# Kernel tuning notes

Hardware: AMD Instinct MI355X
Metric: run time of the kernel (lower is better)

Reference implementation:

```python
import jax, jax.numpy as jnp
import numpy as np

NEG = -1e9  # large negative for masked logits (TRT uses dtype min)

def _rotate_every_two(x):
    # pairs (x0,x1) -> (-x1, x0), interleaved along last dim
    xr = x.reshape(*x.shape[:-1], -1, 2)
    rot = jnp.stack([-xr[..., 1], xr[..., 0]], axis=-1)
    return rot.reshape(x.shape)

def _apply_rope(x, cos, sin):
    # rot_dim == cos.shape[-1]; here it equals the full inner dim
    rot_dim = cos.shape[-1]
    x_rot, x_pass = x[..., :rot_dim], x[..., rot_dim:]
    x_rot = x_rot * cos + _rotate_every_two(x_rot) * sin
    return jnp.concatenate([x_rot, x_pass], axis=-1) if x_pass.shape[-1] else x_rot

def setup_inputs() -> dict:
    key = jax.random.key(0)
    ks = jax.random.split(key, 12)
    B, N, D_MODEL, H, DH = 2, 2048, 1024, 16, 64
    INNER = H * DH
    x = jax.random.normal(ks[0], (B, N, D_MODEL), dtype=jnp.float32)
    # rope angles: build realistic cos/sin tables repeated per head
    pos = jnp.arange(N, dtype=jnp.float32)
    inv = 1.0 / (10000.0 ** (jnp.arange(0, DH, 2, dtype=jnp.float32) / DH))
    ang = pos[:, None] * inv[None, :]              # [N, DH/2]
    ang = jnp.repeat(ang, 2, axis=-1)              # [N, DH] interleaved pairs
    ang = jnp.tile(ang, (1, H))                    # [N, INNER]
    rope_cos = jnp.broadcast_to(jnp.cos(ang)[None], (B, N, INNER)).astype(jnp.float32)
    rope_sin = jnp.broadcast_to(jnp.sin(ang)[None], (B, N, INNER)).astype(jnp.float32)
    input_lengths = jax.random.randint(ks[1], (B,), N // 2, N + 1, dtype=jnp.int32)
    s = 1.0 / np.sqrt(D_MODEL)
    Wq = jax.random.normal(ks[2], (D_MODEL, INNER), dtype=jnp.float32) * s
    bq = jnp.zeros((INNER,), jnp.float32)
    Wk = jax.random.normal(ks[3], (D_MODEL, INNER), dtype=jnp.float32) * s
    bk = jnp.zeros((INNER,), jnp.float32)
    Wv = jax.random.normal(ks[4], (D_MODEL, INNER), dtype=jnp.float32) * s
    bv = jnp.zeros((INNER,), jnp.float32)
    Wo = jax.random.normal(ks[5], (INNER, D_MODEL), dtype=jnp.float32) * (1.0 / np.sqrt(INNER))
    bo = jnp.zeros((D_MODEL,), jnp.float32)
    return {"x": x, "rope_cos": rope_cos, "rope_sin": rope_sin,
            "input_lengths": input_lengths,
            "Wq": Wq, "bq": bq, "Wk": Wk, "bk": bk, "Wv": Wv, "bv": bv,
            "Wo": Wo, "bo": bo}

def reference(x, rope_cos, rope_sin, input_lengths, Wq, bq, Wk, bk, Wv, bv, Wo, bo):
    B, N, _ = x.shape
    H, DH = 16, 64
    q = x @ Wq + bq
    k = x @ Wk + bk
    v = x @ Wv + bv
    q = _apply_rope(q, rope_cos, rope_sin)
    k = _apply_rope(k, rope_cos, rope_sin)
    # split heads: [B,N,H,DH] -> [B,H,N,DH]
    q = q.reshape(B, N, H, DH).transpose(0, 2, 1, 3)
    k = k.reshape(B, N, H, DH).transpose(0, 2, 1, 3)
    v = v.reshape(B, N, H, DH).transpose(0, 2, 1, 3)
    # NOTE: faithful to the non-plugin source path, q is NOT pre-scaled
    scores = jnp.einsum('bhqd,bhkd->bhqk', q, k)
    key_mask = jnp.arange(N)[None, :] < input_lengths[:, None]  # [B,N]
    scores = scores + jnp.where(key_mask, 0.0, NEG).astype(scores.dtype)[:, None, None, :]
    probs = jax.nn.softmax(scores, axis=-1)
    ctx = jnp.einsum('bhqk,bhkd->bhqd', probs, v)  # [B,H,N,DH]
    ctx = ctx.transpose(0, 2, 1, 3).reshape(B, N, H * DH)
    out = ctx @ Wo + bo
    out = out * key_mask[..., None].astype(out.dtype)
    return out
```

## Files before the change

kernel.cpp:

```cpp
#include <hip/hip_runtime.h>
#include <hip/hip_bf16.h>


typedef __fp16 fp16x2 __attribute__((ext_vector_type(2)));
typedef _Float16 f16x8 __attribute__((ext_vector_type(8)));
typedef float f32x4 __attribute__((ext_vector_type(4)));
typedef float f32x16 __attribute__((ext_vector_type(16)));

#define NEGBIG (-1.0e9f)

__device__ inline f32x4 mfma16(f16x8 a, f16x8 b, f32x4 c) {
  return __builtin_amdgcn_mfma_f32_16x16x32_f16(a, b, c, 0, 0, 0);
}
__device__ inline f32x16 mfma32(f16x8 a, f16x8 b, f32x16 c) {
  return __builtin_amdgcn_mfma_f32_32x32x16_f16(a, b, c, 0, 0, 0);
}

__device__ inline void gload16(const void* g, void* l) {
  __builtin_amdgcn_global_load_lds(
      (const __attribute__((address_space(1))) void*)g,
      (__attribute__((address_space(3))) void*)l, 16, 0, 0);
}

__device__ inline unsigned pk2u(float a, float b) {
  union { fp16x2 h; unsigned u; } x;
  x.h = __builtin_amdgcn_cvt_pkrtz(a, b);
  return x.u;
}

__device__ inline float max3f(float a, float b, float c) {
  float d;
  asm("v_max3_f32 %0, %1, %2, %3" : "=v"(d) : "v"(a), "v"(b), "v"(c));
  return d;
}

__global__ __launch_bounds__(256) void prep_kernel(
    const float* __restrict__ x, const float* __restrict__ Wq,
    const float* __restrict__ Wk, const float* __restrict__ Wv,
    const float* __restrict__ Wo, const float* __restrict__ rc,
    const float* __restrict__ rs, _Float16* __restrict__ xh,
    _Float16* __restrict__ wt, float* __restrict__ rc2,
    float* __restrict__ rs2) {
  __shared__ float tile[32][33];
  const int z = blockIdx.z;
  const int tx = threadIdx.x, ty = threadIdx.y;
  if (z == 4) {
    const int bid = blockIdx.y * 32 + blockIdx.x;
    const int t = ty * 32 + tx;
#pragma unroll
    for (int i = 0; i < 4; ++i) {
      const int o = bid * 1024 + i * 256 + t;
      const float4 v = ((const float4*)x)[o];
      union { _Float16 h[4]; short4 s; } u;
      u.h[0] = (_Float16)v.x; u.h[1] = (_Float16)v.y;
      u.h[2] = (_Float16)v.z; u.h[3] = (_Float16)v.w;
      ((short4*)xh)[o] = u.s;
    }
    return;
  }
  if (z == 5) {
    const int bid = blockIdx.y * 32 + blockIdx.x;
    const int idx = bid * 256 + ty * 32 + tx;
    if (idx < 131072) {
      const int n = idx >> 6, d = idx & 63;
      rc2[idx] = rc[(size_t)n * 1024 + d];
      rs2[idx] = rs[(size_t)n * 1024 + d];
    }
    return;
  }
  const float* W = (z == 0) ? Wq : (z == 1) ? Wk : (z == 2) ? Wv : Wo;
  _Float16* dh = wt + (size_t)z * 1024 * 1024;
  const int j0 = blockIdx.x * 32, k0 = blockIdx.y * 32;
  for (int i = ty; i < 32; i += 8)
    tile[i][tx] = W[(size_t)(k0 + i) * 1024 + j0 + tx];
  __syncthreads();
  for (int i = ty; i < 32; i += 8)
    dh[(size_t)(j0 + i) * 1024 + k0 + tx] = (_Float16)tile[tx][i];
}

__global__ __launch_bounds__(512) void gemm256_kernel(
    const _Float16* __restrict__ A, const _Float16* __restrict__ B,
    const float* __restrict__ bias0, const float* __restrict__ bias1,
    const float* __restrict__ bias2, const float* __restrict__ ropeC,
    const float* __restrict__ ropeS, _Float16* __restrict__ outQK,
    _Float16* __restrict__ outVT) {
  __shared__ __align__(16) char lds[131072];
  const int t = threadIdx.x;
  const int lane = t & 63, w = t >> 6;
  const int wr = w >> 2, wc = w & 3;
  const int fr = lane & 15, fg = lane >> 4;
  const int bid = blockIdx.x;
  const int wgid = (bid & 7) * 24 + (bid >> 3);
  const int mtile = wgid & 15, ntile = wgid >> 4;

  const int srw = t >> 3;
  const int ss8 = (((t & 7) ^ (srw & 7)) << 3);
  const size_t aRow = (size_t)(mtile * 256 + srw) * 1024 + ss8;
  const size_t bRow = (size_t)(ntile * 256 + srw) * 1024 + ss8;
  const int t16 = t * 16;

  f32x4 acc[8][4];
#pragma unroll
  for (int i = 0; i < 8; ++i)
#pragma unroll
    for (int j = 0; j < 4; ++j) {
      acc[i][j][0] = 0.f; acc[i][j][1] = 0.f; acc[i][j][2] = 0.f; acc[i][j][3] = 0.f;
    }

#define G256(c, kt_) do { \
    const size_t kc = (size_t)(kt_) * 64; \
    char* ab = lds + (c) * 32768 + t16; \
    char* bb = lds + 65536 + (c) * 32768 + t16; \
    gload16(A + aRow + kc, ab); \
    gload16(A + aRow + kc + 65536, ab + 8192); \
    gload16(A + aRow + kc + 131072, ab + 16384); \
    gload16(A + aRow + kc + 196608, ab + 24576); \
    gload16(B + bRow + kc, bb); \
    gload16(B + bRow + kc + 65536, bb + 8192); \
    gload16(B + bRow + kc + 131072, bb + 16384); \
    gload16(B + bRow + kc + 196608, bb + 24576); \
  } while (0)

  G256(0, 0);
  for (int kt = 0; kt < 16; ++kt) {
    const int cur = kt & 1;
    if (kt < 15) {
      G256(cur ^ 1, kt + 1);
      asm volatile("s_waitcnt vmcnt(8)" ::: "memory");
    } else {
      asm volatile("s_waitcnt vmcnt(0)" ::: "memory");
    }
    __builtin_amdgcn_s_barrier();

    const char* La = lds + cur * 32768;
    const char* Lb = lds + 65536 + cur * 32768;
    const int swz = (fr & 7) << 4;
#pragma unroll
    for (int kk = 0; kk < 2; ++kk) {
      const int ko = (kk * 64 + fg * 16) ^ swz;
      f16x8 af[8], bf[4];
#pragma unroll
      for (int mi = 0; mi < 8; ++mi)
        af[mi] = *(const f16x8*)(La + (wr * 128 + mi * 16 + fr) * 128 + ko);
#pragma unroll
      for (int ni = 0; ni < 4; ++ni)
        bf[ni] = *(const f16x8*)(Lb + (wc * 64 + ni * 16 + fr) * 128 + ko);
      __builtin_amdgcn_s_setprio(1);
#pragma unroll
      for (int mi = 0; mi < 8; ++mi)
#pragma unroll
        for (int ni = 0; ni < 4; ++ni)
          acc[mi][ni] = mfma16(af[mi], bf[ni], acc[mi][ni]);
      __builtin_amdgcn_s_setprio(0);
    }
    asm volatile("" ::: "memory");
    __builtin_amdgcn_s_barrier();
  }
#undef G256

  const int rowbase = mtile * 256 + wr * 128;
  const int colbase = ntile * 256 + wc * 64;
  const int which = colbase >> 10;

  if (which < 2) {
    const float* bias = which ? bias1 : bias0;
    const int hh = (colbase >> 6) & 15;
    const int b = rowbase >> 11;
    const int nbase = rowbase & 2047;
    _Float16* lslab = (_Float16*)lds + w * 1152;
    const char* cslab = (const char*)lslab;
    _Float16* qkbase = outQK + (size_t)((which * 2 + b) * 16 + hh) * 2048 * 64;
    const int rrow = lane >> 2;
    const int rqo = (lane & 3) * 32;
#pragma unroll
    for (int mi = 0; mi < 8; ++mi) {
#pragma unroll
      for (int ni = 0; ni < 4; ++ni) {
        const int dd = ni * 16 + fr;
        const float bv = bias[hh * 64 + dd];
#pragma unroll
        for (int r = 0; r < 4; ++r) {
          const int n = nbase + mi * 16 + fg * 4 + r;
          float val = acc[mi][ni][r] + bv;
          float part = __shfl_xor(val, 1);
          const int ro = n * 64 + dd;
          const float c = ropeC[ro], s = ropeS[ro];
          float rot = (fr & 1) ? (val * c + part * s) : (val * c - part * s);
          if (!which) rot *= 1.44269504f;
          lslab[(fg * 4 + r) * 72 + dd] = (_Float16)rot;
        }
      }
      asm volatile("" ::: "memory");
      const uint4 v0 = *(const uint4*)(cslab + rrow * 144 + rqo);
      const uint4 v1 = *(const uint4*)(cslab + rrow * 144 + rqo + 16);
      _Float16* gdst =
          qkbase + (size_t)(nbase + mi * 16 + rrow) * 64 + (lane & 3) * 16;
      *(uint4*)gdst = v0;
      *(uint4*)(gdst + 8) = v1;
      asm volatile("" ::: "memory");
    }
  } else {
#pragma unroll
    for (int ni = 0; ni < 4; ++ni) {
      const int gcol = colbase + ni * 16 + fr;
      const int jj = gcol & 1023;
      const int hh = jj >> 6, dd = jj & 63;
      const float bv = bias2[jj];
#pragma unroll
      for (int mi = 0; mi < 8; ++mi) {
        const int n0 = rowbase + mi * 16 + fg * 4;
        const int b = n0 >> 11, n = n0 & 2047;
        union { _Float16 h[4]; short4 s4; } u;
#pragma unroll
        for (int r = 0; r < 4; ++r) u.h[r] = (_Float16)(acc[mi][ni][r] + bv);
        *(short4*)(outVT + ((size_t)(b * 16 + hh) * 64 + dd) * 2048 + n) = u.s4;
      }
    }
  }
}

__global__ __launch_bounds__(512) void gemm_out_kernel(
    const _Float16* __restrict__ A, const _Float16* __restrict__ B,
    const float* __restrict__ bias0, const int* __restrict__ lens,
    float* __restrict__ outF) {
  __shared__ __align__(16) char lds[65536];
  const int t = threadIdx.x;
  const int lane = t & 63, w = t >> 6;
  const int wr = w >> 1, wc = w & 1;
  const int fr = lane & 15, fg = lane >> 4;
  const int bid = blockIdx.x;
  const int wgid = (bid & 7) * 32 + (bid >> 3);
  const int mtile = wgid & 31, ntile = wgid >> 5;

  const int srw = t >> 3;
  const int ss8 = (((t & 7) ^ (srw & 7)) << 3);
  const size_t aRow = (size_t)(mtile * 128 + srw) * 1024 + ss8;
  const size_t bRow = (size_t)(ntile * 128 + srw) * 1024 + ss8;
  const int t16 = t * 16;

  f32x4 acc[2][4];
#pragma unroll
  for (int i = 0; i < 2; ++i)
#pragma unroll
    for (int j = 0; j < 4; ++j) {
      acc[i][j][0] = 0.f; acc[i][j][1] = 0.f; acc[i][j][2] = 0.f; acc[i][j][3] = 0.f;
    }

#define GOUT(c, kt_) do { \
    const size_t kc = (size_t)(kt_) * 64; \
    char* ab = lds + (c) * 16384 + t16; \
    char* bb = lds + 32768 + (c) * 16384 + t16; \
    gload16(A + aRow + kc, ab); \
    gload16(A + aRow + kc + 65536, ab + 8192); \
    gload16(B + bRow + kc, bb); \
    gload16(B + bRow + kc + 65536, bb + 8192); \
  } while (0)

  GOUT(0, 0);
  for (int kt = 0; kt < 16; ++kt) {
    const int cur = kt & 1;
    if (kt < 15) {
      GOUT(cur ^ 1, kt + 1);
      asm volatile("s_waitcnt vmcnt(4)" ::: "memory");
    } else {
      asm volatile("s_waitcnt vmcnt(0)" ::: "memory");
    }
    __builtin_amdgcn_s_barrier();

    const char* La = lds + cur * 16384;
    const char* Lb = lds + 32768 + cur * 16384;
    const int swz = (fr & 7) << 4;
#pragma unroll
    for (int kk = 0; kk < 2; ++kk) {
      const int ko = (kk * 64 + fg * 16) ^ swz;
      f16x8 af[2], bf[4];
#pragma unroll
      for (int mi = 0; mi < 2; ++mi)
        af[mi] = *(const f16x8*)(La + (wr * 32 + mi * 16 + fr) * 128 + ko);
#pragma unroll
      for (int ni = 0; ni < 4; ++ni)
        bf[ni] = *(const f16x8*)(Lb + (wc * 64 + ni * 16 + fr) * 128 + ko);
      __builtin_amdgcn_s_setprio(1);
#pragma unroll
      for (int mi = 0; mi < 2; ++mi)
#pragma unroll
        for (int ni = 0; ni < 4; ++ni)
          acc[mi][ni] = mfma16(af[mi], bf[ni], acc[mi][ni]);
      __builtin_amdgcn_s_setprio(0);
    }
    asm volatile("" ::: "memory");
    __builtin_amdgcn_s_barrier();
  }
#undef GOUT

  const int rowbase = mtile * 128 + wr * 32;
  const int colbase = ntile * 128 + wc * 64;
  const int b = rowbase >> 11;
  const int len = lens[b];
#pragma unroll
  for (int ni = 0; ni < 4; ++ni) {
    const int gcol = colbase + ni * 16 + fr;
    const float bv = bias0[gcol];
#pragma unroll
    for (int mi = 0; mi < 2; ++mi) {
#pragma unroll
      for (int r = 0; r < 4; ++r) {
        const int m = rowbase + mi * 16 + fg * 4 + r;
        const int n = m & 2047;
        float val = acc[mi][ni][r] + bv;
        if (n >= len) val = 0.f;
        outF[(size_t)m * 1024 + gcol] = val;
      }
    }
  }
}

__global__ __launch_bounds__(256, 4) void attn_kernel(
    const _Float16* __restrict__ qk, const _Float16* __restrict__ vt,
    const int* __restrict__ lens, unsigned* __restrict__ po,
    float2* __restrict__ ml) {
  __shared__ __align__(16) char lds[32768];
  const int t = threadIdx.x;
  const int w = t >> 6, lane = t & 63;
  const int lq = lane & 31, hi = lane >> 5;
  const int gid = blockIdx.x;
  const int xcd = gid & 7, idx = gid >> 3;
  const int qtile = idx & 15;
  const int c = ((idx >> 4) << 3) + xcd;
  const int bh = c >> 2, seg = c & 3;
  const int b = bh >> 4, h = bh & 15;
  const int len = lens[b];
  const int q0w = qtile * 128 + w * 32;
  const size_t qoff = (size_t)(b * 16 + h) * 2048 * 64;
  const size_t koff = (size_t)((2 + b) * 16 + h) * 2048 * 64;
  const size_t voff = (size_t)(b * 16 + h) * 64 * 2048;

  f16x8 qf[4];
#pragma unroll
  for (int ks = 0; ks < 4; ++ks)
    qf[ks] = *(const f16x8*)(qk + qoff + (size_t)(q0w + lq) * 64 + ks * 16 + hi * 8);

  const int srow = t >> 3;
  const int ss = (t & 7) ^ (srow & 7);
  const size_t kg = koff + (size_t)srow * 64 + ss * 8;
  const int vd = srow + ((ss >> 2) << 5);
  const size_t vg = voff + (size_t)vd * 2048 + (ss & 3) * 8;

  f32x16 o0, o1;
#pragma unroll
  for (int i = 0; i < 16; ++i) { o0[i] = 0.f; o1[i] = 0.f; }
  float mrun = 0.f, lsum = 0.f;

  fp16x2 ones2;
  ones2[0] = (__fp16)1.0f; ones2[1] = (__fp16)1.0f;

#define STAGE(bi, tile0) do { \
    char* dst = lds + (bi) * 16384 + t * 16; \
    const size_t kk = (size_t)(tile0) * 2048; \
    gload16(qk + kg + kk, dst); \
    gload16(qk + kg + kk + 2048, dst + 4096); \
    gload16(vt + vg + (tile0) * 32, dst + 8192); \
    gload16(vt + vg + (tile0) * 32 + 32, dst + 12288); \
  } while (0)

  const int nkb = (len + 31) >> 5;
  const int tb0 = (nkb * seg) >> 2;
  const int tb1 = (nkb * (seg + 1)) >> 2;
  const int nst = (tb1 - tb0 + 1) >> 1;

  STAGE(0, tb0);

  for (int st = 0; st < nst; ++st) {
    const int cur = st & 1;
    if (st + 1 < nst) {
      STAGE(cur ^ 1, tb0 + (st + 1) * 2);
      asm volatile("s_waitcnt vmcnt(4)" ::: "memory");
    } else {
      asm volatile("s_waitcnt vmcnt(0)" ::: "memory");
    }
    __builtin_amdgcn_s_barrier();

    const char* Bb = lds + cur * 16384;
    const int rsw = (lq & 7) << 4;

#pragma unroll
    for (int ch = 0; ch < 2; ++ch) {
      const int kb = tb0 + st * 2 + ch;
      if (kb < tb1) {
        const char* Kb = Bb + ch * 4096;
        const char* Vb = Bb + 8192 + ch * 4096;

        f32x16 s0;
        const float nm = -mrun;
#pragma unroll
        for (int i = 0; i < 16; ++i) s0[i] = nm;
        __builtin_amdgcn_s_setprio(1);
#pragma unroll
        for (int ks = 0; ks < 4; ++ks) {
          const f16x8 kf =
              *(const f16x8*)(Kb + lq * 128 + ((ks * 32 + hi * 16) ^ rsw));
          s0 = mfma32(kf, qf[ks], s0);
        }
        __builtin_amdgcn_s_setprio(0);

        if (kb == nkb - 1 && (len & 31)) {
#pragma unroll
          for (int r = 0; r < 16; ++r) {
            const int key = kb * 32 + (r & 3) + ((r >> 2) << 3) + hi * 4;
            if (key >= len) s0[r] = NEGBIG;
          }
        }

        const float m0 = max3f(s0[0], s0[1], s0[2]);
        const float m1 = max3f(s0[3], s0[4], s0[5]);
        const float m2 = max3f(s0[6], s0[7], s0[8]);
        const float m3 = max3f(s0[9], s0[10], s0[11]);
        const float m4 = max3f(s0[12], s0[13], s0[14]);
        float mx = fmaxf(max3f(m0, m1, m2), max3f(m3, m4, s0[15]));
        mx = fmaxf(mx, __shfl_xor(mx, 32));

        const bool first = (kb == tb0);
        if (first || !__all(mx <= 8.f)) {
          const float delta = first ? mx : fmaxf(mx, 0.f);
          const float scq = __builtin_amdgcn_exp2f(-delta);
          mrun += delta;
          lsum *= scq;
          float sc[16];
#pragma unroll
          for (int r = 0; r < 16; ++r)
            sc[r] = __shfl(scq, (r & 3) + ((r >> 2) << 3) + hi * 4);
#pragma unroll
          for (int r = 0; r < 16; ++r) { o0[r] *= sc[r]; o1[r] *= sc[r]; }
#pragma unroll
          for (int i = 0; i < 16; ++i) s0[i] -= delta;
        }

        unsigned W[8];
#pragma unroll
        for (int u = 0; u < 4; ++u) {
          const float p0 = __builtin_amdgcn_exp2f(s0[4 * u + 0]);
          const float p1 = __builtin_amdgcn_exp2f(s0[4 * u + 1]);
          const float p2 = __builtin_amdgcn_exp2f(s0[4 * u + 2]);
          const float p3 = __builtin_amdgcn_exp2f(s0[4 * u + 3]);
          W[2 * u] = pk2u(p0, p1);
          W[2 * u + 1] = pk2u(p2, p3);
        }
        float ps = 0.f;
#pragma unroll
        for (int i = 0; i < 8; ++i) {
          union { unsigned u; fp16x2 h; } x; x.u = W[i];
          ps = __builtin_amdgcn_fdot2(x.h, ones2, ps, false);
        }
        ps += __shfl_xor(ps, 32);
        lsum += ps;

        __builtin_amdgcn_s_setprio(1);
#pragma unroll
        for (int ks = 0; ks < 2; ++ks) {
          const unsigned w0 = W[4 * ks + 0], w1 = W[4 * ks + 1];
          const unsigned w2 = W[4 * ks + 2], w3 = W[4 * ks + 3];
          const unsigned sendA = hi ? w0 : w2;
          const unsigned sendB = hi ? w1 : w3;
          const unsigned recvA = __shfl_xor(sendA, 32);
          const unsigned recvB = __shfl_xor(sendB, 32);
          union { unsigned u[4]; f16x8 v; } af;
          af.u[0] = hi ? recvA : w0;
          af.u[1] = hi ? recvB : w1;
          af.u[2] = hi ? w2 : recvA;
          af.u[3] = hi ? w3 : recvB;
          const int g0 = ks * 2 + hi;
          const f16x8 v0f = *(const f16x8*)(Vb + lq * 128 + ((g0 << 4) ^ rsw));
          const f16x8 v1f =
              *(const f16x8*)(Vb + lq * 128 + (((g0 + 4) << 4) ^ rsw));
          o0 = mfma32(af.v, v0f, o0);
          o1 = mfma32(af.v, v1f, o1);
        }
        __builtin_amdgcn_s_setprio(0);
      }
    }

    asm volatile("" ::: "memory");
    __builtin_amdgcn_s_barrier();
  }
#undef STAGE

  const size_t rowbase = (size_t)bh * 2048 + q0w;
  const float li = 1.f / lsum;
  unsigned* pod = po + ((size_t)seg * 65536 + rowbase) * 32;
#pragma unroll
  for (int r = 0; r < 16; ++r) {
    const int qr = (r & 3) + ((r >> 2) << 3) + hi * 4;
    const float lr = __shfl(li, qr);
    pod[qr * 32 + lq] = pk2u(o0[r] * lr, o1[r] * lr);
  }
  if (hi == 0) {
    float2 v; v.x = mrun; v.y = lsum;
    ml[(size_t)seg * 65536 + rowbase + lq] = v;
  }
}

__global__ __launch_bounds__(256) void combine_kernel(
    const unsigned* __restrict__ po, const float2* __restrict__ ml,
    _Float16* __restrict__ ctx) {
  const int tid = blockIdx.x * 256 + threadIdx.x;
  const int row = tid >> 5, dg = tid & 31;
  const float2 a0 = ml[row];
  const float2 a1 = ml[65536 + row];
  const float2 a2 = ml[131072 + row];
  const float2 a3 = ml[196608 + row];
  const float m = fmaxf(fmaxf(a0.x, a1.x), fmaxf(a2.x, a3.x));
  const float w0 = a0.y * __builtin_amdgcn_exp2f(a0.x - m);
  const float w1 = a1.y * __builtin_amdgcn_exp2f(a1.x - m);
  const float w2 = a2.y * __builtin_amdgcn_exp2f(a2.x - m);
  const float w3 = a3.y * __builtin_amdgcn_exp2f(a3.x - m);
  const float inv = 1.f / (w0 + w1 + w2 + w3);
  float acc0 = 0.f, acc1 = 0.f;
  const float f[4] = {w0 * inv, w1 * inv, w2 * inv, w3 * inv};
#pragma unroll
  for (int s = 0; s < 4; ++s) {
    union { unsigned u; fp16x2 h; } x;
    x.u = po[((size_t)s * 65536 + row) * 32 + dg];
    acc0 += f[s] * (float)x.h[0];
    acc1 += f[s] * (float)x.h[1];
  }
  const int bh = row >> 11, n = row & 2047, b = bh >> 4, h = bh & 15;
  _Float16* dst = ctx + ((size_t)(b * 2048 + n) * 1024 + h * 64);
  dst[dg] = (_Float16)acc0;
  dst[dg + 32] = (_Float16)acc1;
}


extern "C" void kernel_launch(void* const* d_in, const int* in_sizes, int n_in,
                              void* d_out, int out_size, void* d_ws, size_t ws_size,
                              hipStream_t stream) {
  const float* x = (const float*)d_in[0];
  const float* rc = (const float*)d_in[1];
  const float* rs = (const float*)d_in[2];
  const int* lens = (const int*)d_in[3];
  const float* Wq = (const float*)d_in[4];
  const float* bq = (const float*)d_in[5];
  const float* Wk = (const float*)d_in[6];
  const float* bk = (const float*)d_in[7];
  const float* Wv = (const float*)d_in[8];
  const float* bv = (const float*)d_in[9];
  const float* Wo = (const float*)d_in[10];
  const float* bo = (const float*)d_in[11];
  float* out = (float*)d_out;

  char* ws = (char*)d_ws;
  const size_t MB = 1024 * 1024;
  _Float16* XH = (_Float16*)(ws + 0);
  _Float16* WT = (_Float16*)(ws + 8 * MB);
  _Float16* QK = (_Float16*)(ws + 16 * MB);
  _Float16* VT = (_Float16*)(ws + 32 * MB);
  _Float16* CTX = (_Float16*)(ws + 40 * MB);
  unsigned* PO = (unsigned*)(ws + 48 * MB);
  float2* ML = (float2*)(ws + 80 * MB);
  float* RC2 = (float*)(ws + 48 * MB);
  float* RS2 = (float*)(ws + 48 * MB + 512 * 1024);

  prep_kernel<<<dim3(32, 32, 6), dim3(32, 8), 0, stream>>>(
      x, Wq, Wk, Wv, Wo, rc, rs, XH, WT, RC2, RS2);
  gemm256_kernel<<<192, 512, 0, stream>>>(XH, WT, bq, bk, bv, RC2, RS2, QK,
                                          VT);
  attn_kernel<<<2048, 256, 0, stream>>>(QK, VT, lens, PO, ML);
  combine_kernel<<<8192, 256, 0, stream>>>(PO, ML, CTX);
  gemm_out_kernel<<<256, 512, 0, stream>>>(CTX, WT + (size_t)3 * 1024 * 1024,
                                           bo, lens, out);
}
```

Before: 139.7 us.

## Load K/V fragments directly from global into registers, dropping LDS staging

The attention kernel no longer stages K and V tiles through a double-buffered LDS ring with barriers. Each wave now reads its own K and V MFMA fragments straight from global memory, prefetching the next K tile into registers one iteration ahead. This removes the LDS traffic and the workgroup barriers. In exchange, the four waves of a block each fetch the same K/V data separately, relying on L1/L2 to absorb it, and V loads are exposed within the iteration.

```diff
diff --git a/kernel.cpp b/kernel.cpp
--- a/kernel.cpp
+++ b/kernel.cpp
@@ -319,7 +319,6 @@
     const _Float16* __restrict__ qk, const _Float16* __restrict__ vt,
     const int* __restrict__ lens, unsigned* __restrict__ po,
     float2* __restrict__ ml) {
-  __shared__ __align__(16) char lds[32768];
   const int t = threadIdx.x;
   const int w = t >> 6, lane = t & 63;
   const int lq = lane & 31, hi = lane >> 5;
@@ -340,11 +339,9 @@
   for (int ks = 0; ks < 4; ++ks)
     qf[ks] = *(const f16x8*)(qk + qoff + (size_t)(q0w + lq) * 64 + ks * 16 + hi * 8);
 
-  const int srow = t >> 3;
-  const int ss = (t & 7) ^ (srow & 7);
-  const size_t kg = koff + (size_t)srow * 64 + ss * 8;
-  const int vd = srow + ((ss >> 2) << 5);
-  const size_t vg = voff + (size_t)vd * 2048 + (ss & 3) * 8;
+  const _Float16* kfb = qk + koff + (size_t)lq * 64 + hi * 8;
+  const _Float16* vb0 = vt + voff + (size_t)lq * 2048;
+  const _Float16* vb1 = vb0 + (size_t)32 * 2048;
 
   f32x16 o0, o1;
 #pragma unroll
@@ -353,136 +350,128 @@
 
   fp16x2 ones2;
   ones2[0] = (__fp16)1.0f; ones2[1] = (__fp16)1.0f;
-
-#define STAGE(bi, tile0) do { \
-    char* dst = lds + (bi) * 16384 + t * 16; \
-    const size_t kk = (size_t)(tile0) * 2048; \
-    gload16(qk + kg + kk, dst); \
-    gload16(qk + kg + kk + 2048, dst + 4096); \
-    gload16(vt + vg + (tile0) * 32, dst + 8192); \
-    gload16(vt + vg + (tile0) * 32 + 32, dst + 12288); \
-  } while (0)
 
   const int nkb = (len + 31) >> 5;
   const int tb0 = (nkb * seg) >> 2;
   const int tb1 = (nkb * (seg + 1)) >> 2;
-  const int nst = (tb1 - tb0 + 1) >> 1;
-
-  STAGE(0, tb0);
-
-  for (int st = 0; st < nst; ++st) {
-    const int cur = st & 1;
-    if (st + 1 < nst) {
-      STAGE(cur ^ 1, tb0 + (st + 1) * 2);
-      asm volatile("s_waitcnt vmcnt(4)" ::: "memory");
-    } else {
-      asm volatile("s_waitcnt vmcnt(0)" ::: "memory");
-    }
-    __builtin_amdgcn_s_barrier();
-
-    const char* Bb = lds + cur * 16384;
-    const int rsw = (lq & 7) << 4;
-
-#pragma unroll
-    for (int ch = 0; ch < 2; ++ch) {
-      const int kb = tb0 + st * 2 + ch;
-      if (kb < tb1) {
-        const char* Kb = Bb + ch * 4096;
-        const char* Vb = Bb + 8192 + ch * 4096;
-
-        f32x16 s0;
-        const float nm = -mrun;
-#pragma unroll
-        for (int i = 0; i < 16; ++i) s0[i] = nm;
-        __builtin_amdgcn_s_setprio(1);
-#pragma unroll
-        for (int ks = 0; ks < 4; ++ks) {
-          const f16x8 kf =
-              *(const f16x8*)(Kb + lq * 128 + ((ks * 32 + hi * 16) ^ rsw));
-          s0 = mfma32(kf, qf[ks], s0);
-        }
-        __builtin_amdgcn_s_setprio(0);
-
-        if (kb == nkb - 1 && (len & 31)) {
-#pragma unroll
-          for (int r = 0; r < 16; ++r) {
-            const int key = kb * 32 + (r & 3) + ((r >> 2) << 3) + hi * 4;
-            if (key >= len) s0[r] = NEGBIG;
-          }
-        }
-
-        const float m0 = max3f(s0[0], s0[1], s0[2]);
-        const float m1 = max3f(s0[3], s0[4], s0[5]);
-        const float m2 = max3f(s0[6], s0[7], s0[8]);
-        const float m3 = max3f(s0[9], s0[10], s0[11]);
-        const float m4 = max3f(s0[12], s0[13], s0[14]);
-        float mx = fmaxf(max3f(m0, m1, m2), max3f(m3, m4, s0[15]));
-        mx = fmaxf(mx, __shfl_xor(mx, 32));
-
-        const bool first = (kb == tb0);
-        if (first || !__all(mx <= 8.f)) {
-          const float delta = first ? mx : fmaxf(mx, 0.f);
-          const float scq = __builtin_amdgcn_exp2f(-delta);
-          mrun += delta;
-          lsum *= scq;
-          float sc[16];
-#pragma unroll
-          for (int r = 0; r < 16; ++r)
-            sc[r] = __shfl(scq, (r & 3) + ((r >> 2) << 3) + hi * 4);
-#pragma unroll
-          for (int r = 0; r < 16; ++r) { o0[r] *= sc[r]; o1[r] *= sc[r]; }
-#pragma unroll
-          for (int i = 0; i < 16; ++i) s0[i] -= delta;
-        }
-
-        unsigned W[8];
-#pragma unroll
-        for (int u = 0; u < 4; ++u) {
-          const float p0 = __builtin_amdgcn_exp2f(s0[4 * u + 0]);
-          const float p1 = __builtin_amdgcn_exp2f(s0[4 * u + 1]);
-          const float p2 = __builtin_amdgcn_exp2f(s0[4 * u + 2]);
-          const float p3 = __builtin_amdgcn_exp2f(s0[4 * u + 3]);
-          W[2 * u] = pk2u(p0, p1);
-          W[2 * u + 1] = pk2u(p2, p3);
-        }
-        float ps = 0.f;
-#pragma unroll
-        for (int i = 0; i < 8; ++i) {
-          union { unsigned u; fp16x2 h; } x; x.u = W[i];
-          ps = __builtin_amdgcn_fdot2(x.h, ones2, ps, false);
-        }
-        ps += __shfl_xor(ps, 32);
-        lsum += ps;
-
-        __builtin_amdgcn_s_setprio(1);
-#pragma unroll
-        for (int ks = 0; ks < 2; ++ks) {
-          const unsigned w0 = W[4 * ks + 0], w1 = W[4 * ks + 1];
-          const unsigned w2 = W[4 * ks + 2], w3 = W[4 * ks + 3];
-          const unsigned sendA = hi ? w0 : w2;
-          const unsigned sendB = hi ? w1 : w3;
-          const unsigned recvA = __shfl_xor(sendA, 32);
-          const unsigned recvB = __shfl_xor(sendB, 32);
-          union { unsigned u[4]; f16x8 v; } af;
-          af.u[0] = hi ? recvA : w0;
-          af.u[1] = hi ? recvB : w1;
-          af.u[2] = hi ? w2 : recvA;
-          af.u[3] = hi ? w3 : recvB;
-          const int g0 = ks * 2 + hi;
-          const f16x8 v0f = *(const f16x8*)(Vb + lq * 128 + ((g0 << 4) ^ rsw));
-          const f16x8 v1f =
-              *(const f16x8*)(Vb + lq * 128 + (((g0 + 4) << 4) ^ rsw));
-          o0 = mfma32(af.v, v0f, o0);
-          o1 = mfma32(af.v, v1f, o1);
-        }
-        __builtin_amdgcn_s_setprio(0);
+
+  f16x8 kn0, kn1, kn2, kn3;
+  {
+    const _Float16* kp = kfb + (size_t)tb0 * 2048;
+    kn0 = *(const f16x8*)(kp);
+    kn1 = *(const f16x8*)(kp + 16);
+    kn2 = *(const f16x8*)(kp + 32);
+    kn3 = *(const f16x8*)(kp + 48);
+  }
+
+  for (int kb = tb0; kb < tb1; ++kb) {
+    const int key0 = kb * 32;
+
+    f32x16 s0;
+    const float nm = -mrun;
+#pragma unroll
+    for (int i = 0; i < 16; ++i) s0[i] = nm;
+    __builtin_amdgcn_s_setprio(1);
+    s0 = mfma32(kn0, qf[0], s0);
+    s0 = mfma32(kn1, qf[1], s0);
+    s0 = mfma32(kn2, qf[2], s0);
+    s0 = mfma32(kn3, qf[3], s0);
+    __builtin_amdgcn_s_setprio(0);
+
+    if (kb + 1 < tb1) {
+      const _Float16* kp = kfb + (size_t)(kb + 1) * 2048;
+      kn0 = *(const f16x8*)(kp);
+      kn1 = *(const f16x8*)(kp + 16);
+      kn2 = *(const f16x8*)(kp + 32);
+      kn3 = *(const f16x8*)(kp + 48);
+    }
+    const f16x8 v00 = *(const f16x8*)(vb0 + key0 + hi * 8);
+    const f16x8 v01 = *(const f16x8*)(vb0 + key0 + 16 + hi * 8);
+    const f16x8 v10 = *(const f16x8*)(vb1 + key0 + hi * 8);
+    const f16x8 v11 = *(const f16x8*)(vb1 + key0 + 16 + hi * 8);
+
+    if (kb == nkb - 1 && (len & 31)) {
+#pragma unroll
+      for (int r = 0; r < 16; ++r) {
+        const int key = key0 + (r & 3) + ((r >> 2) << 3) + hi * 4;
+        if (key >= len) s0[r] = NEGBIG;
       }
     }
 
-    asm volatile("" ::: "memory");
-    __builtin_amdgcn_s_barrier();
-  }
-#undef STAGE
+    const float m0 = max3f(s0[0], s0[1], s0[2]);
+    const float m1 = max3f(s0[3], s0[4], s0[5]);
+    const float m2 = max3f(s0[6], s0[7], s0[8]);
+    const float m3 = max3f(s0[9], s0[10], s0[11]);
+    const float m4 = max3f(s0[12], s0[13], s0[14]);
+    float mx = fmaxf(max3f(m0, m1, m2), max3f(m3, m4, s0[15]));
+    mx = fmaxf(mx, __shfl_xor(mx, 32));
+
+    const bool first = (kb == tb0);
+    if (first || !__all(mx <= 8.f)) {
+      const float delta = first ? mx : fmaxf(mx, 0.f);
+      const float scq = __builtin_amdgcn_exp2f(-delta);
+      mrun += delta;
+      lsum *= scq;
+      float sc[16];
+#pragma unroll
+      for (int r = 0; r < 16; ++r)
+        sc[r] = __shfl(scq, (r & 3) + ((r >> 2) << 3) + hi * 4);
+#pragma unroll
+      for (int r = 0; r < 16; ++r) { o0[r] *= sc[r]; o1[r] *= sc[r]; }
+#pragma unroll
+      for (int i = 0; i < 16; ++i) s0[i] -= delta;
+    }
+
+    unsigned W[8];
+#pragma unroll
+    for (int u = 0; u < 4; ++u) {
+      const float p0 = __builtin_amdgcn_exp2f(s0[4 * u + 0]);
+      const float p1 = __builtin_amdgcn_exp2f(s0[4 * u + 1]);
+      const float p2 = __builtin_amdgcn_exp2f(s0[4 * u + 2]);
+      const float p3 = __builtin_amdgcn_exp2f(s0[4 * u + 3]);
+      W[2 * u] = pk2u(p0, p1);
+      W[2 * u + 1] = pk2u(p2, p3);
+    }
+    float ps = 0.f;
+#pragma unroll
+    for (int i = 0; i < 8; ++i) {
+      union { unsigned u; fp16x2 h; } x; x.u = W[i];
+      ps = __builtin_amdgcn_fdot2(x.h, ones2, ps, false);
+    }
+    ps += __shfl_xor(ps, 32);
+    lsum += ps;
+
+    __builtin_amdgcn_s_setprio(1);
+    {
+      const unsigned w0 = W[0], w1 = W[1], w2 = W[2], w3 = W[3];
+      const unsigned sendA = hi ? w0 : w2;
+      const unsigned sendB = hi ? w1 : w3;
+      const unsigned recvA = __shfl_xor(sendA, 32);
+      const unsigned recvB = __shfl_xor(sendB, 32);
+      union { unsigned u[4]; f16x8 v; } af;
+      af.u[0] = hi ? recvA : w0;
+      af.u[1] = hi ? recvB : w1;
+      af.u[2] = hi ? w2 : recvA;
+      af.u[3] = hi ? w3 : recvB;
+      o0 = mfma32(af.v, v00, o0);
+      o1 = mfma32(af.v, v10, o1);
+    }
+    {
+      const unsigned w0 = W[4], w1 = W[5], w2 = W[6], w3 = W[7];
+      const unsigned sendA = hi ? w0 : w2;
+      const unsigned sendB = hi ? w1 : w3;
+      const unsigned recvA = __shfl_xor(sendA, 32);
+      const unsigned recvB = __shfl_xor(sendB, 32);
+      union { unsigned u[4]; f16x8 v; } af;
+      af.u[0] = hi ? recvA : w0;
+      af.u[1] = hi ? recvB : w1;
+      af.u[2] = hi ? w2 : recvA;
+      af.u[3] = hi ? w3 : recvB;
+      o0 = mfma32(af.v, v01, o0);
+      o1 = mfma32(af.v, v11, o1);
+    }
+    __builtin_amdgcn_s_setprio(0);
+  }
 
   const size_t rowbase = (size_t)bh * 2048 + q0w;
   const float li = 1.f / lsum;
```

After: 198.7 us. 42.2% more time.
